# Performance work log

Hardware: AMD Instinct MI355X
Metric: run time of the kernel (lower is better)

## Reference

```python
import jax, jax.numpy as jnp
import numpy as np

N_EMBD = 512
N_HEAD = 8


def setup_inputs() -> dict:
    key = jax.random.key(0)
    k_x, k_aw, k_ab, k_pw, k_pb = jax.random.split(key, 5)
    B, T, E = 4, 2048, N_EMBD
    s = 1.0 / np.sqrt(E)
    return {
        "x": jax.random.normal(k_x, (B, T, E), dtype=jnp.float32),
        # torch Linear weight is [out, in]; store transposed for x @ W
        "c_attn_w": jax.random.uniform(k_aw, (E, 3 * E), jnp.float32, -s, s),
        "c_attn_b": jax.random.uniform(k_ab, (3 * E,), jnp.float32, -s, s),
        "c_proj_w": jax.random.uniform(k_pw, (E, E), jnp.float32, -s, s),
        "c_proj_b": jax.random.uniform(k_pb, (E,), jnp.float32, -s, s),
    }


def reference(x, c_attn_w, c_attn_b, c_proj_w, c_proj_b):
    B, T, E = x.shape
    H = N_HEAD
    D = E // H
    qkv = x @ c_attn_w + c_attn_b                      # [B,T,3E]
    q, k, v = jnp.split(qkv, 3, axis=2)
    # [B,T,E] -> [B,H,T,D]
    q = q.reshape(B, T, H, D).transpose(0, 2, 1, 3)
    k = k.reshape(B, T, H, D).transpose(0, 2, 1, 3)
    v = v.reshape(B, T, H, D).transpose(0, 2, 1, 3)
    scale = 1.0 / np.sqrt(D).astype(np.float32)
    scores = jnp.einsum("bhqd,bhkd->bhqk", q, k) * scale
    causal = jnp.tril(jnp.ones((T, T), dtype=bool))    # [T,T]
    scores = jnp.where(causal, scores, -jnp.inf)
    attn = jax.nn.softmax(scores, axis=-1)             # [B,H,T,T]
    y = jnp.einsum("bhqk,bhkd->bhqd", attn, v)         # [B,H,T,D]
    y = y.transpose(0, 2, 1, 3).reshape(B, T, E)
    return y @ c_proj_w + c_proj_b
```

## Files before the change

### kernel.cpp

```cpp
#include <hip/hip_runtime.h>
#include <math.h>

#define N_EMBD 512
#define N_HEAD 8
#define SEQ_T  2048
#define BATCH  4
#define QK_LD  1024

typedef __attribute__((ext_vector_type(8))) short bf16x8;
typedef __attribute__((ext_vector_type(4))) float f32x4;

#define CL 0.18033688f

__device__ __forceinline__ unsigned short f2bf(float f) {
    union { float f; unsigned int u; } x; x.f = f;
    return (unsigned short)((x.u + 0x7FFFu + ((x.u >> 16) & 1u)) >> 16);
}
__device__ __forceinline__ unsigned pack_trunc(float a, float b) {
    union { float f; unsigned u; } x, y; x.f = a; y.f = b;
    return __builtin_amdgcn_perm(y.u, x.u, 0x07060302u);
}
__device__ __forceinline__ bf16x8 scale_frag(bf16x8 v, float c) {
    bf16x8 r;
    #pragma unroll
    for (int i = 0; i < 8; ++i) {
        union { unsigned u; float f; } x;
        x.u = ((unsigned)(unsigned short)v[i]) << 16;
        r[i] = (short)f2bf(x.f * c);
    }
    return r;
}

__device__ __forceinline__ void gl_lds16(const void* g, void* s) {
    __builtin_amdgcn_global_load_lds(
        (const __attribute__((address_space(1))) void*)g,
        (__attribute__((address_space(3))) void*)s, 16, 0, 0);
}

__global__ __launch_bounds__(256) void prep(
    const float* __restrict__ w1, unsigned short* __restrict__ w1t,
    const float* __restrict__ w2, unsigned short* __restrict__ w2t)
{
    __shared__ float t[32][33];
    const int bx = blockIdx.x, tid = threadIdx.x;
    const float* W; unsigned short* Wt; int N, tt, nb;
    if (bx < 768) { tt = bx;       W = w1; Wt = w1t; N = 1536; nb = 48; }
    else          { tt = bx - 768; W = w2; Wt = w2t; N = 512;  nb = 16; }
    const int n0 = (tt % nb) * 32, k0 = (tt / nb) * 32;
    const int tx = tid & 31, ty = tid >> 5;
    #pragma unroll
    for (int i = 0; i < 4; ++i)
        t[ty + i * 8][tx] = W[(size_t)(k0 + ty + i * 8) * N + n0 + tx];
    __syncthreads();
    #pragma unroll
    for (int i = 0; i < 4; ++i)
        Wt[(size_t)(n0 + ty + i * 8) * 512 + k0 + tx] = f2bf(t[tx][ty + i * 8]);
}

template <int BM, int BN, bool CVT_A, int OMODE>
__global__ __launch_bounds__(256) void gemm_mfma(
    const void* __restrict__ Asrc,
    const unsigned short* __restrict__ Bt,
    const float* __restrict__ bias,
    void* __restrict__ C, unsigned short* __restrict__ Cv,
    int N, int K, int xcdRows)
{
    constexpr int WMT = BM / 32, WNT = BN / 32;
    constexpr int SA = BM * 8 / 256, SB = BN * 8 / 256;
    __shared__ unsigned short SM[BM * 64 + BN * 64];
    unsigned short* As = SM;
    unsigned short* Bs = SM + BM * 64;

    const int tid  = threadIdx.x;
    const int wave = tid >> 6, lane = tid & 63;
    const int low  = lane & 15, quad = lane >> 4;
    const int wm   = (wave & 1) * (BM / 2), wn = (wave >> 1) * (BN / 2);

    const int xcd    = blockIdx.x & 7;
    const int within = blockIdx.x >> 3;
    const int rowBlk = xcd * xcdRows + (within % xcdRows);
    const int colBlk = within / xcdRows;
    const int row0 = rowBlk * BM, col0 = colBlk * BN;

    size_t a_src[SA]; int a_dst[SA];
    #pragma unroll
    for (int s = 0; s < SA; ++s) {
        const int p = tid + 256 * s;
        const int m = p >> 3, q = p & 7;
        a_src[s] = (size_t)(row0 + m) * K + q * 8;
        a_dst[s] = m * 64 + (q ^ (m & 7)) * 8;
    }
    size_t b_src[SB]; int b_dst[SB];
    #pragma unroll
    for (int s = 0; s < SB; ++s) {
        const int p = tid + 256 * s;
        const int m = p >> 3, q = p & 7;
        b_src[s] = (size_t)(col0 + m) * K + q * 8;
        b_dst[s] = m * 64 + (q ^ (m & 7)) * 8;
    }

    f32x4 acc[WMT][WNT];
    #pragma unroll
    for (int i = 0; i < WMT; ++i)
        #pragma unroll
        for (int j = 0; j < WNT; ++j) acc[i][j] = (f32x4){0.f, 0.f, 0.f, 0.f};

    bf16x8 ar[SA], br[SB];
    const float*          af32 = (const float*)Asrc;
    const unsigned short* a16  = (const unsigned short*)Asrc;

    #pragma unroll
    for (int s = 0; s < SA; ++s) {
        if (CVT_A) {
            const float4 f0 = *(const float4*)(af32 + a_src[s]);
            const float4 f1 = *(const float4*)(af32 + a_src[s] + 4);
            union { uint4 v; bf16x8 h; } u;
            u.v.x = pack_trunc(f0.x, f0.y); u.v.y = pack_trunc(f0.z, f0.w);
            u.v.z = pack_trunc(f1.x, f1.y); u.v.w = pack_trunc(f1.z, f1.w);
            ar[s] = u.h;
        } else {
            ar[s] = *(const bf16x8*)(a16 + a_src[s]);
        }
    }
    #pragma unroll
    for (int s = 0; s < SB; ++s) br[s] = *(const bf16x8*)(Bt + b_src[s]);

    const int NIT = K >> 6;
    for (int it = 0; it < NIT; ++it) {
        __syncthreads();
        #pragma unroll
        for (int s = 0; s < SA; ++s) *(bf16x8*)&As[a_dst[s]] = ar[s];
        #pragma unroll
        for (int s = 0; s < SB; ++s) *(bf16x8*)&Bs[b_dst[s]] = br[s];
        __syncthreads();

        if (it + 1 < NIT) {
            const int ko = (it + 1) * 64;
            #pragma unroll
            for (int s = 0; s < SA; ++s) {
                if (CVT_A) {
                    const float4 f0 = *(const float4*)(af32 + a_src[s] + ko);
                    const float4 f1 = *(const float4*)(af32 + a_src[s] + ko + 4);
                    union { uint4 v; bf16x8 h; } u;
                    u.v.x = pack_trunc(f0.x, f0.y); u.v.y = pack_trunc(f0.z, f0.w);
                    u.v.z = pack_trunc(f1.x, f1.y); u.v.w = pack_trunc(f1.z, f1.w);
                    ar[s] = u.h;
                } else {
                    ar[s] = *(const bf16x8*)(a16 + a_src[s] + ko);
                }
            }
            #pragma unroll
            for (int s = 0; s < SB; ++s) br[s] = *(const bf16x8*)(Bt + b_src[s] + ko);
        }

        #pragma unroll
        for (int h = 0; h < 2; ++h) {
            bf16x8 af[WMT], bfr[WNT];
            #pragma unroll
            for (int t = 0; t < WMT; ++t)
                af[t] = *(const bf16x8*)
                    &As[(wm + t * 16 + low) * 64 + (((h * 4 + quad) ^ (low & 7)) * 8)];
            #pragma unroll
            for (int t = 0; t < WNT; ++t)
                bfr[t] = *(const bf16x8*)
                    &Bs[(wn + t * 16 + low) * 64 + (((h * 4 + quad) ^ (low & 7)) * 8)];
            #pragma unroll
            for (int i = 0; i < WMT; ++i)
                #pragma unroll
                for (int j = 0; j < WNT; ++j)
                    acc[i][j] = __builtin_amdgcn_mfma_f32_16x16x32_bf16(
                        af[i], bfr[j], acc[i][j], 0, 0, 0);
        }
    }

    float bv[WNT];
    #pragma unroll
    for (int j = 0; j < WNT; ++j) bv[j] = bias[col0 + wn + j * 16 + low];

    const bool isV = (OMODE == 2) && (col0 >= 1024);
    if (isV) {
        unsigned short (*Cs)[130] = (unsigned short (*)[130])SM;
        const int bI = row0 >> 11;
        const int t0 = row0 & 2047;
        const int dloc = tid >> 2, sub = tid & 3;
        __syncthreads();
        #pragma unroll
        for (int p = 0; p < 2; ++p) {
            if ((wave >> 1) == p) {
                #pragma unroll
                for (int i = 0; i < WMT; ++i)
                    #pragma unroll
                    for (int j = 0; j < WNT; ++j)
                        #pragma unroll
                        for (int r = 0; r < 4; ++r)
                            Cs[j * 16 + low][wm + i * 16 + quad * 4 + r] =
                                f2bf(acc[i][j][r] + bv[j]);
            }
            __syncthreads();
            const int dglob = col0 - 1024 + p * 64 + dloc;
            unsigned short* vb =
                Cv + (((size_t)(bI * 512 + dglob)) << 11) + t0 + sub * 8;
            #pragma unroll
            for (int e = 0; e < 4; ++e)
                *(bf16x8*)(vb + e * 32) = *(const bf16x8*)&Cs[dloc][e * 32 + sub * 8];
            __syncthreads();
        }
    } else {
        #pragma unroll
        for (int i = 0; i < WMT; ++i)
            #pragma unroll
            for (int r = 0; r < 4; ++r) {
                const int row = row0 + wm + i * 16 + quad * 4 + r;
                #pragma unroll
                for (int j = 0; j < WNT; ++j) {
                    const int col = col0 + wn + j * 16 + low;
                    const float v = acc[i][j][r] + bv[j];
                    if (OMODE == 0)
                        ((float*)C)[(size_t)row * N + col] = v;
                    else if (OMODE == 1)
                        ((unsigned short*)C)[(size_t)row * N + col] = f2bf(v);
                    else
                        ((unsigned short*)C)[(size_t)row * QK_LD + col] = f2bf(v);
                }
            }
    }
}

template<bool MASK>
__device__ __forceinline__ void qk_step(
    const bf16x8 k00, const bf16x8 k01, const bf16x8 k10, const bf16x8 k11,
    const bf16x8 (&qf)[2][2], bf16x8 (&pf)[2], float (&lp)[2],
    const int qrel0, const int koffb)
{
    #pragma unroll
    for (int qb = 0; qb < 2; ++qb) {
        f32x4 s0 = (f32x4){0.f, 0.f, 0.f, 0.f};
        f32x4 s1 = (f32x4){0.f, 0.f, 0.f, 0.f};
        s0 = __builtin_amdgcn_mfma_f32_16x16x32_bf16(k00, qf[qb][0], s0, 0, 0, 0);
        s0 = __builtin_amdgcn_mfma_f32_16x16x32_bf16(k01, qf[qb][1], s0, 0, 0, 0);
        s1 = __builtin_amdgcn_mfma_f32_16x16x32_bf16(k10, qf[qb][0], s1, 0, 0, 0);
        s1 = __builtin_amdgcn_mfma_f32_16x16x32_bf16(k11, qf[qb][1], s1, 0, 0, 0);
        float p[8];
        #pragma unroll
        for (int r = 0; r < 4; ++r) {
            float v0 = s0[r], v1 = s1[r];
            if (MASK) {
                const int qrel = qrel0 + qb * 16;
                if (koffb + r     > qrel) v0 = -1e30f;
                if (koffb + r + 4 > qrel) v1 = -1e30f;
            }
            p[r]     = __builtin_amdgcn_exp2f(v0);
            p[r + 4] = __builtin_amdgcn_exp2f(v1);
        }
        #pragma unroll
        for (int e = 0; e < 8; ++e) {
            union { float f; unsigned u; } c; c.f = p[e];
            c.u &= 0xFFFF0000u; p[e] = c.f;
        }
        lp[qb] += ((p[0] + p[1]) + (p[2] + p[3])) + ((p[4] + p[5]) + (p[6] + p[7]));
        union { uint4 v; bf16x8 h; } u;
        u.v.x = pack_trunc(p[0], p[1]); u.v.y = pack_trunc(p[2], p[3]);
        u.v.z = pack_trunc(p[4], p[5]); u.v.w = pack_trunc(p[6], p[7]);
        pf[qb] = u.h;
    }
}

__global__ __launch_bounds__(256, 2) void attn_mfma(
    const unsigned short* __restrict__ qk,
    const unsigned short* __restrict__ vT,
    unsigned short* __restrict__ y)
{
    const int bh  = blockIdx.x & 31;
    const int pa  = blockIdx.x >> 5;
    const int b   = bh >> 3, h = bh & 7;
    const int qA0 = pa * 64;
    const int qB0 = (31 - pa) * 64;
    const int nA  = pa + 1, nB = 32 - pa;
    const int tid = threadIdx.x;
    const int wave = tid >> 6, lane = tid & 63;
    const int low  = lane & 15, quad = lane >> 4;
    const int kh   = wave & 1, qh = wave >> 1;

    __shared__ char smem[34816];
    unsigned short* KsB = (unsigned short*)smem;
    unsigned short* VsB = (unsigned short*)smem + 8192;

    const size_t base = (size_t)b * SEQ_T * QK_LD + h * 64;
    const unsigned short* qp = qk + base;
    const unsigned short* kp = qk + base + 512;
    const unsigned short* vp = vT + ((size_t)(b * 512 + h * 64) << 11);

    bf16x8 qf[2][2][2];
    #pragma unroll
    for (int s = 0; s < 2; ++s) {
        const int q0 = (s ? qB0 : qA0) + qh * 32;
        #pragma unroll
        for (int qb = 0; qb < 2; ++qb) {
            const size_t qr = (size_t)(q0 + qb * 16 + low) * QK_LD;
            #pragma unroll
            for (int dh = 0; dh < 2; ++dh)
                qf[s][qb][dh] = scale_frag(
                    *(const bf16x8*)(qp + qr + dh * 32 + quad * 8), CL);
        }
    }

    const int r8 = lane >> 3, s8 = lane & 7;
    const unsigned short* ksrc[2]; const unsigned short* vsrc[2]; int dst[2];
    #pragma unroll
    for (int ii = 0; ii < 2; ++ii) {
        const int hs = (r8 & 3) | (ii << 2);
        ksrc[ii] = kp + (size_t)(wave * 16 + ii * 8 + r8) * QK_LD + (s8 ^ hs) * 8;
        vsrc[ii] = vp + ((size_t)(wave * 16 + ii * 8 + r8) << 11) + (s8 ^ hs) * 8;
        dst[ii]  = (wave * 16 + ii * 8) * 64;
    }

    const int hkv = (low & 3) | (((low >> 2) & 1) << 2);
    const int hvv = (low & 3) | ((low >> 3) << 2);
    const int krow0 = kh * 32 + ((low >> 2) << 3) + (low & 3);
    const int koffK[2][2] = {
        { krow0 * 64 + ((quad    ) ^ hkv) * 8, krow0 * 64 + ((quad + 4) ^ hkv) * 8 },
        { (krow0+4)*64 + ((quad  ) ^ hkv) * 8, (krow0+4)*64 + ((quad + 4) ^ hkv) * 8 } };
    int voff[4];
    #pragma unroll
    for (int t = 0; t < 4; ++t)
        voff[t] = (t * 16 + low) * 64 + ((kh * 4 + quad) ^ hvv) * 8;
    const int koffb = kh * 32 + quad * 8;

    #pragma unroll
    for (int ii = 0; ii < 2; ++ii) {
        gl_lds16(ksrc[ii], KsB + dst[ii]);
        gl_lds16(vsrc[ii], VsB + dst[ii]);
    }

    f32x4 o[2][2][4];
    #pragma unroll
    for (int s = 0; s < 2; ++s)
        #pragma unroll
        for (int qb = 0; qb < 2; ++qb)
            #pragma unroll
            for (int t = 0; t < 4; ++t) o[s][qb][t] = (f32x4){0.f, 0.f, 0.f, 0.f};
    float lp[2][2] = {{0.f, 0.f}, {0.f, 0.f}};

    __syncthreads();

    for (int kc = 0; kc < nB; ++kc) {
        const int cur = kc & 1;
        if (kc + 1 < nB) {
            const size_t kadv = (size_t)(kc + 1) * 64 * QK_LD;
            const int    vadv = (kc + 1) * 64;
            const int    db   = (cur ^ 1) * 4096;
            #pragma unroll
            for (int ii = 0; ii < 2; ++ii) {
                gl_lds16(ksrc[ii] + kadv, KsB + db + dst[ii]);
                gl_lds16(vsrc[ii] + vadv, VsB + db + dst[ii]);
            }
        }

        const unsigned short* Kc = KsB + cur * 4096;
        const unsigned short* Vc = VsB + cur * 4096;
        bf16x8 kf[2][2], vf[4];
        #pragma unroll
        for (int kt = 0; kt < 2; ++kt)
            #pragma unroll
            for (int dh = 0; dh < 2; ++dh)
                kf[kt][dh] = *(const bf16x8*)&Kc[koffK[kt][dh]];
        #pragma unroll
        for (int t = 0; t < 4; ++t)
            vf[t] = *(const bf16x8*)&Vc[voff[t]];

        const int kc64 = kc * 64;
        bf16x8 pA[2], pB[2];
        const bool doA = (kc < nA);
        if (doA) {
            const int qrelA = qA0 + qh * 32 + low - kc64;
            if (kc == nA - 1)
                qk_step<true >(kf[0][0], kf[0][1], kf[1][0], kf[1][1], qf[0], pA, lp[0], qrelA, koffb);
            else
                qk_step<false>(kf[0][0], kf[0][1], kf[1][0], kf[1][1], qf[0], pA, lp[0], qrelA, koffb);
        }
        {
            const int qrelB = qB0 + qh * 32 + low - kc64;
            if (kc == nB - 1)
                qk_step<true >(kf[0][0], kf[0][1], kf[1][0], kf[1][1], qf[1], pB, lp[1], qrelB, koffb);
            else
                qk_step<false>(kf[0][0], kf[0][1], kf[1][0], kf[1][1], qf[1], pB, lp[1], qrelB, koffb);
        }

        if (doA) {
            #pragma unroll
            for (int t = 0; t < 4; ++t) {
                o[0][0][t] = __builtin_amdgcn_mfma_f32_16x16x32_bf16(pA[0], vf[t], o[0][0][t], 0, 0, 0);
                o[0][1][t] = __builtin_amdgcn_mfma_f32_16x16x32_bf16(pA[1], vf[t], o[0][1][t], 0, 0, 0);
            }
        }
        #pragma unroll
        for (int t = 0; t < 4; ++t) {
            o[1][0][t] = __builtin_amdgcn_mfma_f32_16x16x32_bf16(pB[0], vf[t], o[1][0][t], 0, 0, 0);
            o[1][1][t] = __builtin_amdgcn_mfma_f32_16x16x32_bf16(pB[1], vf[t], o[1][1][t], 0, 0, 0);
        }

        __syncthreads();
    }

    float* oB = (float*)smem;
    float* lB = (float*)(smem + 33792);

    #pragma unroll
    for (int s = 0; s < 2; ++s)
        #pragma unroll
        for (int qb = 0; qb < 2; ++qb) {
            float v = lp[s][qb];
            v += __shfl_xor(v, 16);
            v += __shfl_xor(v, 32);
            if (quad == 0) lB[(kh * 2 + qh) * 64 + (s * 2 + qb) * 16 + low] = v;
        }
    if (kh == 1) {
        #pragma unroll
        for (int s = 0; s < 2; ++s)
            #pragma unroll
            for (int qb = 0; qb < 2; ++qb)
                #pragma unroll
                for (int t = 0; t < 4; ++t)
                    #pragma unroll
                    for (int r = 0; r < 4; ++r)
                        oB[qh * 4224 + ((s * 2 + qb) * 16 + quad * 4 + r) * 66
                           + low + t * 16] = o[s][qb][t][r];
    }
    __syncthreads();
    if (kh == 0) {
        #pragma unroll
        for (int s = 0; s < 2; ++s) {
            const int q0 = (s ? qB0 : qA0) + qh * 32;
            #pragma unroll
            for (int qb = 0; qb < 2; ++qb) {
                #pragma unroll
                for (int r = 0; r < 4; ++r) {
                    const int ri = (s * 2 + qb) * 16 + quad * 4 + r;
                    const float l = lB[qh * 64 + ri] + lB[128 + qh * 64 + ri];
                    const float rl = 1.f / l;
                    const int qrow = q0 + qb * 16 + quad * 4 + r;
                    unsigned short* yp =
                        y + (size_t)(b * SEQ_T + qrow) * N_EMBD + h * 64 + low;
                    #pragma unroll
                    for (int t = 0; t < 4; ++t)
                        yp[t * 16] = f2bf(
                            (o[s][qb][t][r] + oB[qh * 4224 + ri * 66 + low + t * 16]) * rl);
                }
            }
        }
    }
}

extern "C" void kernel_launch(void* const* d_in, const int* in_sizes, int n_in,
                              void* d_out, int out_size, void* d_ws, size_t ws_size,
                              hipStream_t stream)
{
    const float* x      = (const float*)d_in[0];
    const float* attn_w = (const float*)d_in[1];
    const float* attn_b = (const float*)d_in[2];
    const float* proj_w = (const float*)d_in[3];
    const float* proj_b = (const float*)d_in[4];
    float*       out    = (float*)d_out;

    char* ws = (char*)d_ws;
    unsigned short* qk_bf = (unsigned short*)(ws);
    unsigned short* vT    = (unsigned short*)(ws + 16777216);
    unsigned short* y_bf  = (unsigned short*)(ws + 25165824);
    unsigned short* w1t   = (unsigned short*)(ws + 33554432);
    unsigned short* w2t   = (unsigned short*)(ws + 35127296);

    prep<<<1024, 256, 0, stream>>>(attn_w, w1t, proj_w, w2t);

    gemm_mfma<128, 128, true, 2><<<dim3(768), 256, 0, stream>>>(
        x, w1t, attn_b, qk_bf, vT, 1536, N_EMBD, 8);

    attn_mfma<<<dim3(512), 256, 0, stream>>>(qk_bf, vT, y_bf);

    gemm_mfma<64, 128, false, 0><<<dim3(512), 256, 0, stream>>>(
        y_bf, w2t, proj_b, out, nullptr, N_EMBD, N_EMBD, 16);
}
```

Before: 134.7 us.

## Split attention blocks into paired 32-row query tiles with doubled grid

Each attention block now handles two 32-row query tiles (one early, one late in the causal range) instead of two 64-row tiles, with each wave pair owning one tile rather than all waves covering both. The grid doubles to 1024 blocks, per-thread accumulators shrink by half, and launch bounds ask for 4 blocks per CU. The aim is better occupancy and load balance with less register pressure. In exchange, the waves on the short tile sit idle while the block streams the long tile's K/V chunks, and K/V traffic per query row roughly doubles.

```diff
diff --git a/kernel.cpp b/kernel.cpp
--- a/kernel.cpp
+++ b/kernel.cpp
@@ -265,23 +265,26 @@
     }
 }
 
-__global__ __launch_bounds__(256, 2) void attn_mfma(
+__global__ __launch_bounds__(256, 4) void attn_mfma(
     const unsigned short* __restrict__ qk,
     const unsigned short* __restrict__ vT,
     unsigned short* __restrict__ y)
 {
     const int bh  = blockIdx.x & 31;
-    const int pa  = blockIdx.x >> 5;
+    const int a   = blockIdx.x >> 5;
     const int b   = bh >> 3, h = bh & 7;
-    const int qA0 = pa * 64;
-    const int qB0 = (31 - pa) * 64;
-    const int nA  = pa + 1, nB = 32 - pa;
+    const int a0  = a * 32;
+    const int b0  = (63 - a) * 32;
+    const int nAt = (a >> 1) + 1;
+    const int nBt = ((63 - a) >> 1) + 1;
     const int tid = threadIdx.x;
     const int wave = tid >> 6, lane = tid & 63;
     const int low  = lane & 15, quad = lane >> 4;
-    const int kh   = wave & 1, qh = wave >> 1;
-
-    __shared__ char smem[34816];
+    const int kh   = wave & 1, sh = wave >> 1;
+    const int qS   = sh ? b0 : a0;
+    const int nSt  = sh ? nBt : nAt;
+
+    __shared__ char smem[32768];
     unsigned short* KsB = (unsigned short*)smem;
     unsigned short* VsB = (unsigned short*)smem + 8192;
 
@@ -290,18 +293,14 @@
     const unsigned short* kp = qk + base + 512;
     const unsigned short* vp = vT + ((size_t)(b * 512 + h * 64) << 11);
 
-    bf16x8 qf[2][2][2];
-    #pragma unroll
-    for (int s = 0; s < 2; ++s) {
-        const int q0 = (s ? qB0 : qA0) + qh * 32;
-        #pragma unroll
-        for (int qb = 0; qb < 2; ++qb) {
-            const size_t qr = (size_t)(q0 + qb * 16 + low) * QK_LD;
-            #pragma unroll
-            for (int dh = 0; dh < 2; ++dh)
-                qf[s][qb][dh] = scale_frag(
-                    *(const bf16x8*)(qp + qr + dh * 32 + quad * 8), CL);
-        }
+    bf16x8 qf[2][2];
+    #pragma unroll
+    for (int qb = 0; qb < 2; ++qb) {
+        const size_t qr = (size_t)(qS + qb * 16 + low) * QK_LD;
+        #pragma unroll
+        for (int dh = 0; dh < 2; ++dh)
+            qf[qb][dh] = scale_frag(
+                *(const bf16x8*)(qp + qr + dh * 32 + quad * 8), CL);
     }
 
     const int r8 = lane >> 3, s8 = lane & 7;
@@ -332,20 +331,18 @@
         gl_lds16(vsrc[ii], VsB + dst[ii]);
     }
 
-    f32x4 o[2][2][4];
-    #pragma unroll
-    for (int s = 0; s < 2; ++s)
-        #pragma unroll
-        for (int qb = 0; qb < 2; ++qb)
-            #pragma unroll
-            for (int t = 0; t < 4; ++t) o[s][qb][t] = (f32x4){0.f, 0.f, 0.f, 0.f};
-    float lp[2][2] = {{0.f, 0.f}, {0.f, 0.f}};
+    f32x4 o[2][4];
+    #pragma unroll
+    for (int qb = 0; qb < 2; ++qb)
+        #pragma unroll
+        for (int t = 0; t < 4; ++t) o[qb][t] = (f32x4){0.f, 0.f, 0.f, 0.f};
+    float lp[2] = {0.f, 0.f};
 
     __syncthreads();
 
-    for (int kc = 0; kc < nB; ++kc) {
+    for (int kc = 0; kc < nBt; ++kc) {
         const int cur = kc & 1;
-        if (kc + 1 < nB) {
+        if (kc + 1 < nBt) {
             const size_t kadv = (size_t)(kc + 1) * 64 * QK_LD;
             const int    vadv = (kc + 1) * 64;
             const int    db   = (cur ^ 1) * 4096;
@@ -356,96 +353,72 @@
             }
         }
 
-        const unsigned short* Kc = KsB + cur * 4096;
-        const unsigned short* Vc = VsB + cur * 4096;
-        bf16x8 kf[2][2], vf[4];
-        #pragma unroll
-        for (int kt = 0; kt < 2; ++kt)
-            #pragma unroll
-            for (int dh = 0; dh < 2; ++dh)
-                kf[kt][dh] = *(const bf16x8*)&Kc[koffK[kt][dh]];
-        #pragma unroll
-        for (int t = 0; t < 4; ++t)
-            vf[t] = *(const bf16x8*)&Vc[voff[t]];
-
-        const int kc64 = kc * 64;
-        bf16x8 pA[2], pB[2];
-        const bool doA = (kc < nA);
-        if (doA) {
-            const int qrelA = qA0 + qh * 32 + low - kc64;
-            if (kc == nA - 1)
-                qk_step<true >(kf[0][0], kf[0][1], kf[1][0], kf[1][1], qf[0], pA, lp[0], qrelA, koffb);
+        if (kc < nSt) {
+            const unsigned short* Kc = KsB + cur * 4096;
+            const unsigned short* Vc = VsB + cur * 4096;
+            bf16x8 kf[2][2], vf[4];
+            #pragma unroll
+            for (int kt = 0; kt < 2; ++kt)
+                #pragma unroll
+                for (int dh = 0; dh < 2; ++dh)
+                    kf[kt][dh] = *(const bf16x8*)&Kc[koffK[kt][dh]];
+            #pragma unroll
+            for (int t = 0; t < 4; ++t)
+                vf[t] = *(const bf16x8*)&Vc[voff[t]];
+
+            bf16x8 pf[2];
+            const int qrel = qS + low - kc * 64;
+            if (kc == nSt - 1)
+                qk_step<true >(kf[0][0], kf[0][1], kf[1][0], kf[1][1], qf, pf, lp, qrel, koffb);
             else
-                qk_step<false>(kf[0][0], kf[0][1], kf[1][0], kf[1][1], qf[0], pA, lp[0], qrelA, koffb);
-        }
-        {
-            const int qrelB = qB0 + qh * 32 + low - kc64;
-            if (kc == nB - 1)
-                qk_step<true >(kf[0][0], kf[0][1], kf[1][0], kf[1][1], qf[1], pB, lp[1], qrelB, koffb);
-            else
-                qk_step<false>(kf[0][0], kf[0][1], kf[1][0], kf[1][1], qf[1], pB, lp[1], qrelB, koffb);
-        }
-
-        if (doA) {
+                qk_step<false>(kf[0][0], kf[0][1], kf[1][0], kf[1][1], qf, pf, lp, qrel, koffb);
+
             #pragma unroll
             for (int t = 0; t < 4; ++t) {
-                o[0][0][t] = __builtin_amdgcn_mfma_f32_16x16x32_bf16(pA[0], vf[t], o[0][0][t], 0, 0, 0);
-                o[0][1][t] = __builtin_amdgcn_mfma_f32_16x16x32_bf16(pA[1], vf[t], o[0][1][t], 0, 0, 0);
-            }
-        }
-        #pragma unroll
-        for (int t = 0; t < 4; ++t) {
-            o[1][0][t] = __builtin_amdgcn_mfma_f32_16x16x32_bf16(pB[0], vf[t], o[1][0][t], 0, 0, 0);
-            o[1][1][t] = __builtin_amdgcn_mfma_f32_16x16x32_bf16(pB[1], vf[t], o[1][1][t], 0, 0, 0);
+                o[0][t] = __builtin_amdgcn_mfma_f32_16x16x32_bf16(pf[0], vf[t], o[0][t], 0, 0, 0);
+                o[1][t] = __builtin_amdgcn_mfma_f32_16x16x32_bf16(pf[1], vf[t], o[1][t], 0, 0, 0);
+            }
         }
 
         __syncthreads();
     }
 
     float* oB = (float*)smem;
-    float* lB = (float*)(smem + 33792);
-
-    #pragma unroll
-    for (int s = 0; s < 2; ++s)
-        #pragma unroll
-        for (int qb = 0; qb < 2; ++qb) {
-            float v = lp[s][qb];
-            v += __shfl_xor(v, 16);
-            v += __shfl_xor(v, 32);
-            if (quad == 0) lB[(kh * 2 + qh) * 64 + (s * 2 + qb) * 16 + low] = v;
-        }
+    float* lB = (float*)(smem + 16896);
+
+    #pragma unroll
+    for (int qb = 0; qb < 2; ++qb) {
+        float v = lp[qb];
+        v += __shfl_xor(v, 16);
+        v += __shfl_xor(v, 32);
+        if (quad == 0) lB[(kh * 2 + sh) * 32 + qb * 16 + low] = v;
+    }
     if (kh == 1) {
         #pragma unroll
-        for (int s = 0; s < 2; ++s)
-            #pragma unroll
-            for (int qb = 0; qb < 2; ++qb)
-                #pragma unroll
-                for (int t = 0; t < 4; ++t)
-                    #pragma unroll
-                    for (int r = 0; r < 4; ++r)
-                        oB[qh * 4224 + ((s * 2 + qb) * 16 + quad * 4 + r) * 66
-                           + low + t * 16] = o[s][qb][t][r];
+        for (int qb = 0; qb < 2; ++qb)
+            #pragma unroll
+            for (int t = 0; t < 4; ++t)
+                #pragma unroll
+                for (int r = 0; r < 4; ++r)
+                    oB[sh * 2112 + (qb * 16 + quad * 4 + r) * 66 + low + t * 16]
+                        = o[qb][t][r];
     }
     __syncthreads();
     if (kh == 0) {
         #pragma unroll
-        for (int s = 0; s < 2; ++s) {
-            const int q0 = (s ? qB0 : qA0) + qh * 32;
-            #pragma unroll
-            for (int qb = 0; qb < 2; ++qb) {
-                #pragma unroll
-                for (int r = 0; r < 4; ++r) {
-                    const int ri = (s * 2 + qb) * 16 + quad * 4 + r;
-                    const float l = lB[qh * 64 + ri] + lB[128 + qh * 64 + ri];
-                    const float rl = 1.f / l;
-                    const int qrow = q0 + qb * 16 + quad * 4 + r;
-                    unsigned short* yp =
-                        y + (size_t)(b * SEQ_T + qrow) * N_EMBD + h * 64 + low;
-                    #pragma unroll
-                    for (int t = 0; t < 4; ++t)
-                        yp[t * 16] = f2bf(
-                            (o[s][qb][t][r] + oB[qh * 4224 + ri * 66 + low + t * 16]) * rl);
-                }
+        for (int qb = 0; qb < 2; ++qb) {
+            #pragma unroll
+            for (int r = 0; r < 4; ++r) {
+                const int ri = qb * 16 + quad * 4 + r;
+                const float l = lB[sh * 32 + ri] + lB[64 + sh * 32 + ri];
+                const float rl = 1.f / l;
+                const int qrow = qS + ri;
+                unsigned short* yp =
+                    y + (size_t)(b * SEQ_T + qrow) * N_EMBD + h * 64 + low;
+                #pragma unroll
+                for (int t = 0; t < 4; ++t)
+                    yp[t * 16] = f2bf(
+                        (o[qb][t][r] + oB[sh * 2112 + ri * 66 + low + t * 16]) * rl);
             }
         }
     }
@@ -474,7 +447,7 @@
     gemm_mfma<128, 128, true, 2><<<dim3(768), 256, 0, stream>>>(
         x, w1t, attn_b, qk_bf, vT, 1536, N_EMBD, 8);
 
-    attn_mfma<<<dim3(512), 256, 0, stream>>>(qk_bf, vT, y_bf);
+    attn_mfma<<<dim3(1024), 256, 0, stream>>>(qk_bf, vT, y_bf);
 
     gemm_mfma<64, 128, false, 0><<<dim3(512), 256, 0, stream>>>(
         y_bf, w2t, proj_b, out, nullptr, N_EMBD, N_EMBD, 16);
```

Measured after the change: 136.0 us. Within noise of the previous version (+1.0%).
